# Kernel tuning notes

Measured on AMD Instinct MI355X. Metric: run time of the kernel, lower is better.

The kernel has to match this reference:

```python
import jax, jax.numpy as jnp
import numpy as np

B = 1
T_DIM, H_DIM, W_DIM = 8, 24, 24          # video canvas (t, h, w)
TT, TH, TW = 2, 8, 8                      # tile sizes
WT, WH, WW = 6, 16, 16                    # window sizes (tokens)
HIDDEN = 1024
HEADS = 16
DH = HIDDEN // HEADS
SEQ = T_DIM * H_DIM * W_DIM               # 4608
NT, NH, NW = T_DIM // TT, H_DIM // TH, W_DIM // TW   # tile grid (4,3,3)
N_TILES = NT * NH * NW                    # 36
TILE = TT * TH * TW                       # 128


def _gather_indices():
    # STA tile mask: kv tile allowed iff |clamp(q_tile, k//2, n-1-k//2) - kv_tile| <= k//2 per axis.
    # Due to the clamp, every query tile attends to exactly the same number of kv tiles,
    # so the block-sparse pattern is a dense gather of shape [N_TILES, K].
    def axis(n, kernel_tiles):
        half = kernel_tiles // 2
        c = np.clip(np.arange(n), half, n - 1 - half)
        return c[:, None] + np.arange(-half, half + 1)[None, :]  # [n, 2*half+1]
    ts = axis(NT, WT // TT)
    hs = axis(NH, WH // TH)
    ws = axis(NW, WW // TW)
    idx = (ts[:, None, None, :, None, None] * NH
           + hs[None, :, None, None, :, None]) * NW \
          + ws[None, None, :, None, None, :]
    return idx.reshape(N_TILES, -1).astype(np.int32)  # [N_TILES, K]


def setup_inputs() -> dict:
    key = jax.random.key(0)
    k1, k2, k3, k4, k5 = jax.random.split(key, 5)
    s = 0.02
    return {
        "hidden_states": jax.random.normal(k1, (B, SEQ, HIDDEN), jnp.float32),
        "q_w": jax.random.normal(k2, (HIDDEN, HIDDEN), jnp.float32) * s,
        "k_w": jax.random.normal(k3, (HIDDEN, HIDDEN), jnp.float32) * s,
        "v_w": jax.random.normal(k4, (HIDDEN, HIDDEN), jnp.float32) * s,
        "o_w": jax.random.normal(k5, (HIDDEN, HIDDEN), jnp.float32) * s,
    }


def _tileize(x):
    # [B, S, HEADS*DH] -> [B, HEADS, N_TILES, TILE, DH] in (t,h,w) tile-major order
    x = x.reshape(B, NT, TT, NH, TH, NW, TW, HEADS, DH)
    x = x.transpose(0, 7, 1, 3, 5, 2, 4, 6, 8)
    return x.reshape(B, HEADS, N_TILES, TILE, DH)


def _untileize(x):
    # [B, HEADS, N_TILES, TILE, DH] -> [B, S, HEADS*DH]
    x = x.reshape(B, HEADS, NT, NH, NW, TT, TH, TW, DH)
    x = x.transpose(0, 2, 5, 3, 6, 4, 7, 1, 8)
    return x.reshape(B, SEQ, HEADS * DH)


def reference(hidden_states, q_w, k_w, v_w, o_w):
    q = _tileize(hidden_states @ q_w.T)
    k = _tileize(hidden_states @ k_w.T)
    v = _tileize(hidden_states @ v_w.T)
    idx = jnp.asarray(_gather_indices())          # [N_TILES, K] (static)
    kk = k[:, :, idx]                              # [B, H, N_TILES, K, TILE, DH]
    vv = v[:, :, idx]
    K = idx.shape[1]
    kk = kk.reshape(B, HEADS, N_TILES, K * TILE, DH)
    vv = vv.reshape(B, HEADS, N_TILES, K * TILE, DH)
    scale = 1.0 / np.sqrt(DH).astype(np.float32)
    scores = jnp.einsum('bhnqd,bhnkd->bhnqk', q * scale, kk)  # [B,H,nT,TILE,K*TILE]
    attn = jax.nn.softmax(scores, axis=-1)
    out = jnp.einsum('bhnqk,bhnkd->bhnqd', attn, vv)
    return _untileize(out) @ o_w.T
```

## Files before the change

kernel.cpp:

```cpp
#include <hip/hip_runtime.h>
#include <math.h>

#define HID 1024
#define NHEADS 16
#define NTILES 36
#define HEADSZ (36*128*64)
#define LOG2E 1.4426950408889634f
#define PLSTRIDE 73728

typedef unsigned short u16;
typedef unsigned int u32;
typedef __attribute__((ext_vector_type(8))) u16 ushort8v;
typedef __attribute__((ext_vector_type(8))) __bf16 bf16x8;
typedef __attribute__((ext_vector_type(16))) float f32x16;
typedef __attribute__((ext_vector_type(4))) u32 u32x4;

__device__ __forceinline__ u32 cvt_pk_bf16(float lo, float hi) {
  u32 r;
  asm("v_cvt_pk_bf16_f32 %0, %1, %2" : "=v"(r) : "v"(lo), "v"(hi));
  return r;
}
__device__ __forceinline__ void permlane32_swap(u32 &a, u32 &b) {
  asm volatile("v_permlane32_swap_b32 %0, %1" : "+v"(a), "+v"(b));
}
__device__ __forceinline__ void gld_lds16(const void* g, void* l) {
  __builtin_amdgcn_global_load_lds((const __attribute__((address_space(1))) u32*)g,
                                   (__attribute__((address_space(3))) u32*)l, 16, 0, 0);
}
__device__ __forceinline__ f32x16 mfma32(bf16x8 a, bf16x8 b, f32x16 c) {
  return __builtin_amdgcn_mfma_f32_32x32x16_bf16(a, b, c, 0, 0, 0);
}
__device__ __forceinline__ u16 bf16r(float x) {
  u32 b = __builtin_bit_cast(u32, x);
  b += 0x7fff + ((b >> 16) & 1);
  return (u16)(b >> 16);
}
__device__ __forceinline__ float bf2f(u16 v) {
  return __builtin_bit_cast(float, (u32)v << 16);
}

struct CastJob { const float* src[5]; u16* dst[5]; int n[5]; };

__global__ __launch_bounds__(256)
void cast_bf16(CastJob j) {
  const int w = blockIdx.y;
  const int n = j.n[w];
  const int i = (blockIdx.x * 256 + threadIdx.x) * 8;
  if (i >= n) return;
  const float4 v0 = *reinterpret_cast<const float4*>(j.src[w] + i);
  const float4 v1 = *reinterpret_cast<const float4*>(j.src[w] + i + 4);
  u32x4 o;
  o.x = cvt_pk_bf16(v0.x, v0.y);
  o.y = cvt_pk_bf16(v0.z, v0.w);
  o.z = cvt_pk_bf16(v1.x, v1.y);
  o.w = cvt_pk_bf16(v1.z, v1.w);
  *reinterpret_cast<u32x4*>(j.dst[w] + i) = o;
}

template<int AMODE, int CMODE, bool QKV, bool DBUF>
__global__ __launch_bounds__(256)
void gemm_mfma(const u16* __restrict__ A, const u16* __restrict__ B,
               void* __restrict__ Cv, float alpha)
{
    __shared__ __align__(16) u16 sm[DBUF ? 2 : 1][2][8192];

    const int tid = threadIdx.x;
    const int wv = tid >> 6, l = tid & 63;
    const int l31 = l & 31, hi = l >> 5;
    const int wm = wv >> 1, wn = wv & 1;
    const int by = blockIdx.y;
    const int n0 = blockIdx.x * 128;
    const float av = (QKV && n0 >= 1024) ? 1.0f : alpha;

    const int tt = by / 9, rem = by % 9, th = rem / 3, tw = rem % 3;
    const int tilebase = tt * 1152 + th * 192 + tw * 8;

    const int lrow = l >> 3;
    const int lslot = l & 7;
    const int sg = (lslot ^ lrow) * 8;
    const u16* aptr[4];
    const u16* bptr[4];
#pragma unroll
    for (int i = 0; i < 4; ++i) {
        const int row = (wv * 4 + i) * 8 + lrow;
        if (AMODE == 0) {
            const int s = tilebase + (row >> 6) * 576 + ((row >> 3) & 7) * 24 + (row & 7);
            aptr[i] = A + (size_t)s * HID + sg;
        } else {
            aptr[i] = A + (size_t)(by * 128 + row) * 64 + sg;
        }
        bptr[i] = B + (size_t)(n0 + row) * HID + sg;
    }

    auto stage = [&](int buf, int kc) {
#pragma unroll
        for (int i = 0; i < 4; ++i) {
            const u16* ga = (AMODE == 0) ? (aptr[i] + kc)
                                         : (aptr[i] + (size_t)(kc >> 6) * HEADSZ);
            gld_lds16(ga, &sm[buf][0][(wv * 4 + i) * 512]);
            gld_lds16(bptr[i] + kc, &sm[buf][1][(wv * 4 + i) * 512]);
        }
    };

    f32x16 acc[2][2];
#pragma unroll
    for (int mb = 0; mb < 2; ++mb)
#pragma unroll
        for (int nb = 0; nb < 2; ++nb)
#pragma unroll
            for (int i = 0; i < 16; ++i) acc[mb][nb][i] = 0.f;

    auto compute = [&](int buf) {
        __builtin_amdgcn_s_setprio(1);
#pragma unroll
        for (int kk = 0; kk < 4; ++kk) {
            bf16x8 af[2], bfr[2];
#pragma unroll
            for (int mb = 0; mb < 2; ++mb) {
                const int row = wm * 64 + mb * 32 + l31;
                af[mb] = *reinterpret_cast<const bf16x8*>(
                    &sm[buf][0][row * 64 + (((kk * 2 + hi) ^ (row & 7)) * 8)]);
            }
#pragma unroll
            for (int nb = 0; nb < 2; ++nb) {
                const int row = wn * 64 + nb * 32 + l31;
                bfr[nb] = *reinterpret_cast<const bf16x8*>(
                    &sm[buf][1][row * 64 + (((kk * 2 + hi) ^ (row & 7)) * 8)]);
            }
#pragma unroll
            for (int mb = 0; mb < 2; ++mb)
#pragma unroll
                for (int nb = 0; nb < 2; ++nb)
                    acc[mb][nb] = mfma32(af[mb], bfr[nb], acc[mb][nb]);
        }
        __builtin_amdgcn_s_setprio(0);
    };

    if (DBUF) {
        stage(0, 0);
        __syncthreads();
        int cur = 0;
        for (int kc = 0; kc < HID; kc += 64) {
            if (kc + 64 < HID) stage(cur ^ 1, kc + 64);
            compute(cur);
            __syncthreads();
            cur ^= 1;
        }
    } else {
        for (int kc = 0; kc < HID; kc += 64) {
            __syncthreads();
            stage(0, kc);
            __syncthreads();
            compute(0);
        }
    }

    if (CMODE == 0) {
        float* C = (float*)Cv;
#pragma unroll
        for (int mb = 0; mb < 2; ++mb)
#pragma unroll
            for (int r = 0; r < 16; ++r) {
                const int m = wm * 64 + mb * 32 + (r & 3) + 8 * (r >> 2) + 4 * hi;
                const int s = tilebase + (m >> 6) * 576 + ((m >> 3) & 7) * 24 + (m & 7);
#pragma unroll
                for (int nb = 0; nb < 2; ++nb) {
                    const int n = n0 + wn * 64 + nb * 32 + l31;
                    C[(size_t)s * HID + n] = acc[mb][nb][r] * av;
                }
            }
    } else {
        u16* C = (u16*)Cv;
#pragma unroll
        for (int mb = 0; mb < 2; ++mb)
#pragma unroll
            for (int rq = 0; rq < 4; ++rq) {
                const int mbase = wm * 64 + mb * 32 + 8 * rq + 4 * hi;
#pragma unroll
                for (int nb = 0; nb < 2; ++nb) {
                    const int n = n0 + wn * 64 + nb * 32 + l31;
                    const int head = n >> 6, dh = n & 63;
                    if (QKV && head >= 32) {
                        u32 w0 = cvt_pk_bf16(acc[mb][nb][rq * 4 + 0], acc[mb][nb][rq * 4 + 1]);
                        u32 w1 = cvt_pk_bf16(acc[mb][nb][rq * 4 + 2], acc[mb][nb][rq * 4 + 3]);
                        *reinterpret_cast<uint2*>(C + (size_t)head * HEADSZ +
                            (size_t)by * 8192 + dh * 128 + mbase) = make_uint2(w0, w1);
                    } else {
#pragma unroll
                        for (int j = 0; j < 4; ++j) {
                            const int m = mbase + j;
                            C[(size_t)head * HEADSZ + (size_t)(by * 128 + m) * 64 + dh] =
                                bf16r(acc[mb][nb][rq * 4 + j] * av);
                        }
                    }
                }
            }
    }
}

__global__ __launch_bounds__(256, 5)
void attn_mfma(const u16* __restrict__ Q, const u16* __restrict__ K,
               const u16* __restrict__ Vt, u16* __restrict__ pO0,
               u16* __restrict__ pO1, float* __restrict__ pl)
{
    __shared__ u16 sm[2][2][4096];

    const int tid = threadIdx.x;
    const int wave = tid >> 6;
    const int lane = tid & 63;
    const int l31 = lane & 31;
    const int hi  = lane >> 5;

    const int logical = (blockIdx.x & 7) * 144 + (blockIdx.x >> 3);
    const int p  = logical & 1;
    const int bt = logical >> 1;
    const int tl = bt % NTILES;
    const int hd = bt / NTILES;
    const size_t headbase = (size_t)hd * HEADSZ;

    const u16* Qg = Q + headbase + (size_t)tl * 8192;
    const u16* Kh = K + headbase;
    const u16* Vh = Vt + headbase;

    bf16x8 qf[4];
    {
        const u16* qrow = Qg + (wave * 32 + l31) * 64 + hi * 8;
#pragma unroll
        for (int ks = 0; ks < 4; ++ks)
            qf[ks] = *reinterpret_cast<const bf16x8*>(qrow + ks * 16);
    }

    const int base_t = (min(max(tl / 9, 1), 2) - 1) * 9;

    const int srow = lane >> 3;
    const int slot = lane & 7;

    auto stage = [&](int i, int bi) {
        const int kt = base_t + i;
        const u16* Kg = Kh + (size_t)kt * 8192 + p * 4096;
        const u16* Vg = Vh + (size_t)kt * 8192 + p * 64;
        u16* dk = &sm[bi][0][0];
        u16* dv = &sm[bi][1][0];
#pragma unroll
        for (int q = 0; q < 2; ++q) {
            const int seg = wave * 2 + q;
            const int key = seg * 8 + srow;
            gld_lds16(Kg + key * 64 + ((slot ^ (key & 7)) * 8), dk + seg * 512);
            const int dh = seg * 8 + srow;
            gld_lds16(Vg + dh * 128 + ((slot ^ (dh & 7)) * 8), dv + seg * 512);
        }
    };

    f32x16 accO0, accO1;
#pragma unroll
    for (int i = 0; i < 16; ++i) { accO0[i] = 0.f; accO1[i] = 0.f; }
    float lsum = 0.f;

    stage(0, 0);
    __syncthreads();

    for (int i = 0; i < 27; ++i) {
        const int cur = i & 1;
        if (i + 1 < 27) stage(i + 1, cur ^ 1);
        const u16* Ksb = &sm[cur][0][0];
        const u16* Vsb = &sm[cur][1][0];

#pragma unroll
        for (int c = 0; c < 2; ++c) {
            f32x16 s;
#pragma unroll
            for (int i2 = 0; i2 < 16; ++i2) s[i2] = 0.f;
            const int kr = c * 32 + l31;
            __builtin_amdgcn_s_setprio(1);
#pragma unroll
            for (int ks = 0; ks < 4; ++ks) {
                bf16x8 a = *reinterpret_cast<const bf16x8*>(
                    Ksb + kr * 64 + (((2 * ks + hi) ^ (kr & 7)) * 8));
                s = mfma32(a, qf[ks], s);
            }
            __builtin_amdgcn_s_setprio(0);

#pragma unroll
            for (int i2 = 0; i2 < 16; ++i2) s[i2] = __builtin_amdgcn_exp2f(s[i2]);

            float ps = 0.f;
#pragma unroll
            for (int i2 = 0; i2 < 16; ++i2) ps += s[i2];
            lsum += ps;

            bf16x8 pb[2];
            {
                u32 a0 = cvt_pk_bf16(s[0], s[1]);
                u32 a1 = cvt_pk_bf16(s[2], s[3]);
                u32 b0 = cvt_pk_bf16(s[4], s[5]);
                u32 b1 = cvt_pk_bf16(s[6], s[7]);
                permlane32_swap(a0, b0);
                permlane32_swap(a1, b1);
                u32x4 w; w.x = a0; w.y = a1; w.z = b0; w.w = b1;
                pb[0] = __builtin_bit_cast(bf16x8, w);
                u32 c0 = cvt_pk_bf16(s[8], s[9]);
                u32 c1 = cvt_pk_bf16(s[10], s[11]);
                u32 d0 = cvt_pk_bf16(s[12], s[13]);
                u32 d1 = cvt_pk_bf16(s[14], s[15]);
                permlane32_swap(c0, d0);
                permlane32_swap(c1, d1);
                u32x4 w2; w2.x = c0; w2.y = c1; w2.z = d0; w2.w = d1;
                pb[1] = __builtin_bit_cast(bf16x8, w2);
            }

            __builtin_amdgcn_s_setprio(1);
#pragma unroll
            for (int k2 = 0; k2 < 2; ++k2) {
                const int sg2 = c * 4 + k2 * 2 + hi;
                bf16x8 v0 = *reinterpret_cast<const bf16x8*>(
                    Vsb + l31 * 64 + ((sg2 ^ (l31 & 7)) * 8));
                accO0 = mfma32(v0, pb[k2], accO0);
                bf16x8 v1 = *reinterpret_cast<const bf16x8*>(
                    Vsb + (32 + l31) * 64 + ((sg2 ^ (l31 & 7)) * 8));
                accO1 = mfma32(v1, pb[k2], accO1);
            }
            __builtin_amdgcn_s_setprio(0);
        }
        __syncthreads();
    }

    lsum += __shfl_xor(lsum, 32);

    u16* Ob = (p ? pO1 : pO0) + ((size_t)bt * 128 + wave * 32 + l31) * 64;
#pragma unroll
    for (int t = 0; t < 4; ++t) {
        u32 p0 = cvt_pk_bf16(accO0[4 * t], accO0[4 * t + 1]);
        u32 p1 = cvt_pk_bf16(accO0[4 * t + 2], accO0[4 * t + 3]);
        *reinterpret_cast<uint2*>(Ob + t * 8 + 4 * hi) = make_uint2(p0, p1);
        u32 q0 = cvt_pk_bf16(accO1[4 * t], accO1[4 * t + 1]);
        u32 q1 = cvt_pk_bf16(accO1[4 * t + 2], accO1[4 * t + 3]);
        *reinterpret_cast<uint2*>(Ob + 32 + t * 8 + 4 * hi) = make_uint2(q0, q1);
    }
    if (hi == 0) pl[p * PLSTRIDE + bt * 128 + wave * 32 + l31] = lsum;
}

__global__ __launch_bounds__(256)
void merge_attn(const u16* __restrict__ pO0, const u16* __restrict__ pO1,
                const float* __restrict__ pl, u16* __restrict__ O)
{
    const int b = blockIdx.x;
    const int tid = threadIdx.x;
    const int row = tid >> 1;
    const int d0 = (tid & 1) * 32;
    const size_t rbase = ((size_t)b * 128 + row) * 64 + d0;
    const float inv = 1.f / (pl[b * 128 + row] + pl[PLSTRIDE + b * 128 + row]);
#pragma unroll
    for (int g = 0; g < 4; ++g) {
        ushort8v a = *reinterpret_cast<const ushort8v*>(pO0 + rbase + g * 8);
        ushort8v c = *reinterpret_cast<const ushort8v*>(pO1 + rbase + g * 8);
        u32 w[4];
#pragma unroll
        for (int h = 0; h < 4; ++h) {
            float f0 = (bf2f(a[2 * h])     + bf2f(c[2 * h]))     * inv;
            float f1 = (bf2f(a[2 * h + 1]) + bf2f(c[2 * h + 1])) * inv;
            w[h] = cvt_pk_bf16(f0, f1);
        }
        u32x4 st; st.x = w[0]; st.y = w[1]; st.z = w[2]; st.w = w[3];
        *reinterpret_cast<u32x4*>(O + rbase + g * 8) = st;
    }
}

extern "C" void kernel_launch(void* const* d_in, const int* in_sizes, int n_in,
                              void* d_out, int out_size, void* d_ws, size_t ws_size,
                              hipStream_t stream) {
    const float* hs = (const float*)d_in[0];
    const float* qw = (const float*)d_in[1];
    const float* kw = (const float*)d_in[2];
    const float* vw = (const float*)d_in[3];
    const float* ow = (const float*)d_in[4];
    float* out = (float*)d_out;

    const size_t TSZ = (size_t)NHEADS * HEADSZ;
    const size_t WSZ = (size_t)HID * HID;
    u16* hsb = (u16*)d_ws;
    u16* wqb = hsb + TSZ;
    u16* wkb = wqb + WSZ;
    u16* wvb = wkb + WSZ;
    u16* wob = wvb + WSZ;
    u16* qb  = wob + WSZ;
    u16* kb  = qb + TSZ;
    u16* vt  = kb + TSZ;
    u16* pO0 = hsb;
    u16* pO1 = vt + TSZ;
    float* pl = (float*)(pO1 + TSZ);
    u16* aob = (u16*)(pl + 2 * PLSTRIDE);

    CastJob cj;
    cj.src[0] = hs; cj.dst[0] = hsb; cj.n[0] = (int)TSZ;
    cj.src[1] = qw; cj.dst[1] = wqb; cj.n[1] = (int)WSZ;
    cj.src[2] = kw; cj.dst[2] = wkb; cj.n[2] = (int)WSZ;
    cj.src[3] = vw; cj.dst[3] = wvb; cj.n[3] = (int)WSZ;
    cj.src[4] = ow; cj.dst[4] = wob; cj.n[4] = (int)WSZ;
    cast_bf16<<<dim3(2304, 5), 256, 0, stream>>>(cj);

    gemm_mfma<0, 1, true, true><<<dim3(24, 36), 256, 0, stream>>>(hsb, wqb, qb, 0.125f * LOG2E);
    attn_mfma<<<NHEADS * NTILES * 2, 256, 0, stream>>>(qb, kb, vt, pO0, pO1, pl);
    merge_attn<<<NHEADS * NTILES, 256, 0, stream>>>(pO0, pO1, pl, aob);
    gemm_mfma<1, 0, false, true><<<dim3(8, 36), 256, 0, stream>>>(aob, wob, out, 1.0f);
}
```

Measured before the change: 158.6 us.

## Split attention waves over query and key halves, reduce partial outputs through LDS

The 4 waves in each attention block are regrouped as a 2x2 grid. Each wave now handles 64 query rows against 32 of the 64 keys in a stage, instead of 32 query rows against all 64 keys. Each K fragment loaded from LDS now feeds two query blocks, and each V fragment feeds two accumulators, which roughly halves per-wave LDS reads per MFMA. The two key-half waves then combine their partial outputs and row sums through an LDS reduction after the loop. In exchange the kernel holds more accumulator and Q registers, drops the occupancy hint from 5 to 3 blocks, and adds an extra barrier and epilogue pass.

```diff
diff --git a/kernel.cpp b/kernel.cpp
--- a/kernel.cpp
+++ b/kernel.cpp
@@ -198,18 +198,21 @@
     }
 }
 
-__global__ __launch_bounds__(256, 5)
+__global__ __launch_bounds__(256, 3)
 void attn_mfma(const u16* __restrict__ Q, const u16* __restrict__ K,
                const u16* __restrict__ Vt, u16* __restrict__ pO0,
                u16* __restrict__ pO1, float* __restrict__ pl)
 {
     __shared__ u16 sm[2][2][4096];
+    __shared__ float lsl[2][2][32];
 
     const int tid = threadIdx.x;
     const int wave = tid >> 6;
     const int lane = tid & 63;
     const int l31 = lane & 31;
     const int hi  = lane >> 5;
+    const int qw  = wave & 1;
+    const int kw  = wave >> 1;
 
     const int logical = (blockIdx.x & 7) * 144 + (blockIdx.x >> 3);
     const int p  = logical & 1;
@@ -222,12 +225,13 @@
     const u16* Kh = K + headbase;
     const u16* Vh = Vt + headbase;
 
-    bf16x8 qf[4];
-    {
-        const u16* qrow = Qg + (wave * 32 + l31) * 64 + hi * 8;
+    bf16x8 qf[2][4];
+#pragma unroll
+    for (int qb = 0; qb < 2; ++qb) {
+        const u16* qrow = Qg + (qw * 64 + qb * 32 + l31) * 64 + hi * 8;
 #pragma unroll
         for (int ks = 0; ks < 4; ++ks)
-            qf[ks] = *reinterpret_cast<const bf16x8*>(qrow + ks * 16);
+            qf[qb][ks] = *reinterpret_cast<const bf16x8*>(qrow + ks * 16);
     }
 
     const int base_t = (min(max(tl / 9, 1), 2) - 1) * 9;
@@ -251,13 +255,19 @@
         }
     };
 
-    f32x16 accO0, accO1;
-#pragma unroll
-    for (int i = 0; i < 16; ++i) { accO0[i] = 0.f; accO1[i] = 0.f; }
-    float lsum = 0.f;
+    f32x16 accO[2][2];
+#pragma unroll
+    for (int dhb = 0; dhb < 2; ++dhb)
+#pragma unroll
+        for (int qb = 0; qb < 2; ++qb)
+#pragma unroll
+            for (int i = 0; i < 16; ++i) accO[dhb][qb][i] = 0.f;
+    float lsum[2] = {0.f, 0.f};
 
     stage(0, 0);
     __syncthreads();
+
+    const int kr = kw * 32 + l31;
 
     for (int i = 0; i < 27; ++i) {
         const int cur = i & 1;
@@ -265,19 +275,22 @@
         const u16* Ksb = &sm[cur][0][0];
         const u16* Vsb = &sm[cur][1][0];
 
-#pragma unroll
-        for (int c = 0; c < 2; ++c) {
+        bf16x8 af[4];
+#pragma unroll
+        for (int ks = 0; ks < 4; ++ks)
+            af[ks] = *reinterpret_cast<const bf16x8*>(
+                Ksb + kr * 64 + (((2 * ks + hi) ^ (kr & 7)) * 8));
+
+        bf16x8 pb[2][2];
+#pragma unroll
+        for (int qb = 0; qb < 2; ++qb) {
             f32x16 s;
 #pragma unroll
             for (int i2 = 0; i2 < 16; ++i2) s[i2] = 0.f;
-            const int kr = c * 32 + l31;
             __builtin_amdgcn_s_setprio(1);
 #pragma unroll
-            for (int ks = 0; ks < 4; ++ks) {
-                bf16x8 a = *reinterpret_cast<const bf16x8*>(
-                    Ksb + kr * 64 + (((2 * ks + hi) ^ (kr & 7)) * 8));
-                s = mfma32(a, qf[ks], s);
-            }
+            for (int ks = 0; ks < 4; ++ks)
+                s = mfma32(af[ks], qf[qb][ks], s);
             __builtin_amdgcn_s_setprio(0);
 
 #pragma unroll
@@ -286,57 +299,99 @@
             float ps = 0.f;
 #pragma unroll
             for (int i2 = 0; i2 < 16; ++i2) ps += s[i2];
-            lsum += ps;
-
-            bf16x8 pb[2];
-            {
-                u32 a0 = cvt_pk_bf16(s[0], s[1]);
-                u32 a1 = cvt_pk_bf16(s[2], s[3]);
-                u32 b0 = cvt_pk_bf16(s[4], s[5]);
-                u32 b1 = cvt_pk_bf16(s[6], s[7]);
-                permlane32_swap(a0, b0);
-                permlane32_swap(a1, b1);
-                u32x4 w; w.x = a0; w.y = a1; w.z = b0; w.w = b1;
-                pb[0] = __builtin_bit_cast(bf16x8, w);
-                u32 c0 = cvt_pk_bf16(s[8], s[9]);
-                u32 c1 = cvt_pk_bf16(s[10], s[11]);
-                u32 d0 = cvt_pk_bf16(s[12], s[13]);
-                u32 d1 = cvt_pk_bf16(s[14], s[15]);
-                permlane32_swap(c0, d0);
-                permlane32_swap(c1, d1);
-                u32x4 w2; w2.x = c0; w2.y = c1; w2.z = d0; w2.w = d1;
-                pb[1] = __builtin_bit_cast(bf16x8, w2);
-            }
-
-            __builtin_amdgcn_s_setprio(1);
-#pragma unroll
-            for (int k2 = 0; k2 < 2; ++k2) {
-                const int sg2 = c * 4 + k2 * 2 + hi;
-                bf16x8 v0 = *reinterpret_cast<const bf16x8*>(
-                    Vsb + l31 * 64 + ((sg2 ^ (l31 & 7)) * 8));
-                accO0 = mfma32(v0, pb[k2], accO0);
-                bf16x8 v1 = *reinterpret_cast<const bf16x8*>(
-                    Vsb + (32 + l31) * 64 + ((sg2 ^ (l31 & 7)) * 8));
-                accO1 = mfma32(v1, pb[k2], accO1);
-            }
-            __builtin_amdgcn_s_setprio(0);
-        }
+            lsum[qb] += ps;
+
+            u32 a0 = cvt_pk_bf16(s[0], s[1]);
+            u32 a1 = cvt_pk_bf16(s[2], s[3]);
+            u32 b0 = cvt_pk_bf16(s[4], s[5]);
+            u32 b1 = cvt_pk_bf16(s[6], s[7]);
+            permlane32_swap(a0, b0);
+            permlane32_swap(a1, b1);
+            u32x4 w; w.x = a0; w.y = a1; w.z = b0; w.w = b1;
+            pb[qb][0] = __builtin_bit_cast(bf16x8, w);
+            u32 c0 = cvt_pk_bf16(s[8], s[9]);
+            u32 c1 = cvt_pk_bf16(s[10], s[11]);
+            u32 d0 = cvt_pk_bf16(s[12], s[13]);
+            u32 d1 = cvt_pk_bf16(s[14], s[15]);
+            permlane32_swap(c0, d0);
+            permlane32_swap(c1, d1);
+            u32x4 w2; w2.x = c0; w2.y = c1; w2.z = d0; w2.w = d1;
+            pb[qb][1] = __builtin_bit_cast(bf16x8, w2);
+        }
+
+        __builtin_amdgcn_s_setprio(1);
+#pragma unroll
+        for (int k2 = 0; k2 < 2; ++k2) {
+            const int sg2 = kw * 4 + k2 * 2 + hi;
+            bf16x8 v0 = *reinterpret_cast<const bf16x8*>(
+                Vsb + l31 * 64 + ((sg2 ^ (l31 & 7)) * 8));
+            bf16x8 v1 = *reinterpret_cast<const bf16x8*>(
+                Vsb + (32 + l31) * 64 + ((sg2 ^ ((32 + l31) & 7)) * 8));
+            accO[0][0] = mfma32(v0, pb[0][k2], accO[0][0]);
+            accO[1][0] = mfma32(v1, pb[0][k2], accO[1][0]);
+            accO[0][1] = mfma32(v0, pb[1][k2], accO[0][1]);
+            accO[1][1] = mfma32(v1, pb[1][k2], accO[1][1]);
+        }
+        __builtin_amdgcn_s_setprio(0);
         __syncthreads();
     }
 
-    lsum += __shfl_xor(lsum, 32);
-
-    u16* Ob = (p ? pO1 : pO0) + ((size_t)bt * 128 + wave * 32 + l31) * 64;
-#pragma unroll
-    for (int t = 0; t < 4; ++t) {
-        u32 p0 = cvt_pk_bf16(accO0[4 * t], accO0[4 * t + 1]);
-        u32 p1 = cvt_pk_bf16(accO0[4 * t + 2], accO0[4 * t + 3]);
-        *reinterpret_cast<uint2*>(Ob + t * 8 + 4 * hi) = make_uint2(p0, p1);
-        u32 q0 = cvt_pk_bf16(accO1[4 * t], accO1[4 * t + 1]);
-        u32 q1 = cvt_pk_bf16(accO1[4 * t + 2], accO1[4 * t + 3]);
-        *reinterpret_cast<uint2*>(Ob + 32 + t * 8 + 4 * hi) = make_uint2(q0, q1);
-    }
-    if (hi == 0) pl[p * PLSTRIDE + bt * 128 + wave * 32 + l31] = lsum;
+    lsum[0] += __shfl_xor(lsum[0], 32);
+    lsum[1] += __shfl_xor(lsum[1], 32);
+
+    float* fs = reinterpret_cast<float*>(&sm[0][0][0]);
+    if (kw == 1) {
+#pragma unroll
+        for (int dhb = 0; dhb < 2; ++dhb)
+#pragma unroll
+            for (int qb = 0; qb < 2; ++qb)
+#pragma unroll
+                for (int r4 = 0; r4 < 4; ++r4) {
+                    const int c = (dhb * 2 + qb) * 4 + r4;
+                    float4 v = make_float4(accO[dhb][qb][4 * r4 + 0],
+                                           accO[dhb][qb][4 * r4 + 1],
+                                           accO[dhb][qb][4 * r4 + 2],
+                                           accO[dhb][qb][4 * r4 + 3]);
+                    *reinterpret_cast<float4*>(&fs[qw * 4096 + c * 256 + lane * 4]) = v;
+                }
+        if (hi == 0) { lsl[qw][0][l31] = lsum[0]; lsl[qw][1][l31] = lsum[1]; }
+    }
+    __syncthreads();
+    if (kw == 0) {
+#pragma unroll
+        for (int dhb = 0; dhb < 2; ++dhb)
+#pragma unroll
+            for (int qb = 0; qb < 2; ++qb)
+#pragma unroll
+                for (int r4 = 0; r4 < 4; ++r4) {
+                    const int c = (dhb * 2 + qb) * 4 + r4;
+                    float4 v = *reinterpret_cast<const float4*>(
+                        &fs[qw * 4096 + c * 256 + lane * 4]);
+                    accO[dhb][qb][4 * r4 + 0] += v.x;
+                    accO[dhb][qb][4 * r4 + 1] += v.y;
+                    accO[dhb][qb][4 * r4 + 2] += v.z;
+                    accO[dhb][qb][4 * r4 + 3] += v.w;
+                }
+        lsum[0] += lsl[qw][0][l31];
+        lsum[1] += lsl[qw][1][l31];
+
+        u16* Ob = (p ? pO1 : pO0) + ((size_t)(bt * 128 + qw * 64)) * 64;
+#pragma unroll
+        for (int qb = 0; qb < 2; ++qb)
+#pragma unroll
+            for (int dhb = 0; dhb < 2; ++dhb)
+#pragma unroll
+                for (int t = 0; t < 4; ++t) {
+                    u32 w0 = cvt_pk_bf16(accO[dhb][qb][4 * t + 0], accO[dhb][qb][4 * t + 1]);
+                    u32 w1 = cvt_pk_bf16(accO[dhb][qb][4 * t + 2], accO[dhb][qb][4 * t + 3]);
+                    *reinterpret_cast<uint2*>(Ob + (qb * 32 + l31) * 64 +
+                                              dhb * 32 + t * 8 + 4 * hi) = make_uint2(w0, w1);
+                }
+        if (hi == 0) {
+            pl[p * PLSTRIDE + bt * 128 + qw * 64 + l31]      = lsum[0];
+            pl[p * PLSTRIDE + bt * 128 + qw * 64 + 32 + l31] = lsum[1];
+        }
+    }
 }
 
 __global__ __launch_bounds__(256)
```

Measured after the change: 197.7 us. +24.7%, slower.

## Fuse split-KV merge into output projection GEMM with smaller M tiles

Applied to the files above, without the earlier changes.

Removes the separate merge_attn kernel and folds the two-partial softmax merge (sum of partials times reciprocal of combined row sums) into the A-operand load of a new output-projection GEMM. The new GEMM reads the per-head partial outputs directly, merges them in registers, writes them to LDS, and uses 64-row tiles giving a 8x72 grid. This avoids one launch and a full intermediate write and read. In exchange the A path now uses plain register loads instead of direct-to-LDS loads, and each block fetches two partial buffers plus row sums for every k-chunk.

```diff
diff --git a/kernel.cpp b/kernel.cpp
--- a/kernel.cpp
+++ b/kernel.cpp
@@ -195,6 +195,126 @@
                     }
                 }
             }
+    }
+}
+
+__global__ __launch_bounds__(256)
+void gemm_out(const u16* __restrict__ P0, const u16* __restrict__ P1,
+              const float* __restrict__ PL, const u16* __restrict__ B,
+              float* __restrict__ C)
+{
+    __shared__ __align__(16) u16 smA[2][4096];
+    __shared__ __align__(16) u16 smB[2][8192];
+
+    const int tid = threadIdx.x;
+    const int wv = tid >> 6, l = tid & 63;
+    const int l31 = l & 31, hi = l >> 5;
+    const int wm = wv >> 1, wn = wv & 1;
+    const int by = blockIdx.y;
+    const int n0 = blockIdx.x * 128;
+
+    const int tile = by >> 1;
+    const int tt = tile / 9, rem = tile % 9, th = rem / 3, tw = rem % 3;
+    const int tilebase = tt * 1152 + th * 192 + tw * 8;
+
+    const int lrow = l >> 3;
+    const int lslot = l & 7;
+    const int sg = (lslot ^ lrow) * 8;
+
+    const u16* bptr[4];
+#pragma unroll
+    for (int i = 0; i < 4; ++i) {
+        const int row = (wv * 4 + i) * 8 + lrow;
+        bptr[i] = B + (size_t)(n0 + row) * HID + sg;
+    }
+    int arow[2];
+#pragma unroll
+    for (int i = 0; i < 2; ++i) arow[i] = (wv * 2 + i) * 8 + lrow;
+
+    auto stageB = [&](int buf, int kc) {
+#pragma unroll
+        for (int i = 0; i < 4; ++i)
+            gld_lds16(bptr[i] + kc, &smB[buf][(wv * 4 + i) * 512]);
+    };
+
+    ushort8v a0[2], a1[2];
+    float ls[2];
+    auto loadA = [&](int kc) {
+        const int head = kc >> 6;
+#pragma unroll
+        for (int i = 0; i < 2; ++i) {
+            const size_t gb = (size_t)head * HEADSZ +
+                              (size_t)(by * 64 + arow[i]) * 64 + sg;
+            a0[i] = *reinterpret_cast<const ushort8v*>(P0 + gb);
+            a1[i] = *reinterpret_cast<const ushort8v*>(P1 + gb);
+            const int pli = head * 4608 + by * 64 + arow[i];
+            ls[i] = PL[pli] + PL[PLSTRIDE + pli];
+        }
+    };
+    auto mergeA = [&](int buf) {
+#pragma unroll
+        for (int i = 0; i < 2; ++i) {
+            const float r = __builtin_amdgcn_rcpf(ls[i]);
+            u32 w[4];
+#pragma unroll
+            for (int h = 0; h < 4; ++h) {
+                float f0 = (bf2f(a0[i][2 * h])     + bf2f(a1[i][2 * h]))     * r;
+                float f1 = (bf2f(a0[i][2 * h + 1]) + bf2f(a1[i][2 * h + 1])) * r;
+                w[h] = cvt_pk_bf16(f0, f1);
+            }
+            u32x4 st; st.x = w[0]; st.y = w[1]; st.z = w[2]; st.w = w[3];
+            *reinterpret_cast<u32x4*>(&smA[buf][(wv * 2 + i) * 512 + l * 8]) = st;
+        }
+    };
+
+    f32x16 acc[2];
+#pragma unroll
+    for (int nb = 0; nb < 2; ++nb)
+#pragma unroll
+        for (int i = 0; i < 16; ++i) acc[nb][i] = 0.f;
+
+    auto compute = [&](int buf) {
+        __builtin_amdgcn_s_setprio(1);
+#pragma unroll
+        for (int kk = 0; kk < 4; ++kk) {
+            const int ar = wm * 32 + l31;
+            bf16x8 af = *reinterpret_cast<const bf16x8*>(
+                &smA[buf][ar * 64 + (((kk * 2 + hi) ^ (ar & 7)) * 8)]);
+#pragma unroll
+            for (int nb = 0; nb < 2; ++nb) {
+                const int brow = wn * 64 + nb * 32 + l31;
+                bf16x8 bf_ = *reinterpret_cast<const bf16x8*>(
+                    &smB[buf][brow * 64 + (((kk * 2 + hi) ^ (brow & 7)) * 8)]);
+                acc[nb] = mfma32(af, bf_, acc[nb]);
+            }
+        }
+        __builtin_amdgcn_s_setprio(0);
+    };
+
+    loadA(0);
+    stageB(0, 0);
+    mergeA(0);
+    __syncthreads();
+    int cur = 0;
+    for (int kc = 0; kc < HID; kc += 64) {
+        const bool more = (kc + 64 < HID);
+        if (more) { loadA(kc + 64); stageB(cur ^ 1, kc + 64); }
+        compute(cur);
+        if (more) mergeA(cur ^ 1);
+        __syncthreads();
+        cur ^= 1;
+    }
+
+#pragma unroll
+    for (int r = 0; r < 16; ++r) {
+        const int m = wm * 32 + (r & 3) + 8 * (r >> 2) + 4 * hi;
+        const int r128 = (by & 1) * 64 + m;
+        const int s = tilebase + (r128 >> 6) * 576 + ((r128 >> 3) & 7) * 24 + (r128 & 7);
+#pragma unroll
+        for (int nb = 0; nb < 2; ++nb) {
+            const int n = n0 + wn * 64 + nb * 32 + l31;
+            C[(size_t)s * HID + n] = acc[nb][r];
+        }
     }
 }
 
@@ -339,32 +459,6 @@
     if (hi == 0) pl[p * PLSTRIDE + bt * 128 + wave * 32 + l31] = lsum;
 }
 
-__global__ __launch_bounds__(256)
-void merge_attn(const u16* __restrict__ pO0, const u16* __restrict__ pO1,
-                const float* __restrict__ pl, u16* __restrict__ O)
-{
-    const int b = blockIdx.x;
-    const int tid = threadIdx.x;
-    const int row = tid >> 1;
-    const int d0 = (tid & 1) * 32;
-    const size_t rbase = ((size_t)b * 128 + row) * 64 + d0;
-    const float inv = 1.f / (pl[b * 128 + row] + pl[PLSTRIDE + b * 128 + row]);
-#pragma unroll
-    for (int g = 0; g < 4; ++g) {
-        ushort8v a = *reinterpret_cast<const ushort8v*>(pO0 + rbase + g * 8);
-        ushort8v c = *reinterpret_cast<const ushort8v*>(pO1 + rbase + g * 8);
-        u32 w[4];
-#pragma unroll
-        for (int h = 0; h < 4; ++h) {
-            float f0 = (bf2f(a[2 * h])     + bf2f(c[2 * h]))     * inv;
-            float f1 = (bf2f(a[2 * h + 1]) + bf2f(c[2 * h + 1])) * inv;
-            w[h] = cvt_pk_bf16(f0, f1);
-        }
-        u32x4 st; st.x = w[0]; st.y = w[1]; st.z = w[2]; st.w = w[3];
-        *reinterpret_cast<u32x4*>(O + rbase + g * 8) = st;
-    }
-}
-
 extern "C" void kernel_launch(void* const* d_in, const int* in_sizes, int n_in,
                               void* d_out, int out_size, void* d_ws, size_t ws_size,
                               hipStream_t stream) {
@@ -388,7 +482,6 @@
     u16* pO0 = hsb;
     u16* pO1 = vt + TSZ;
     float* pl = (float*)(pO1 + TSZ);
-    u16* aob = (u16*)(pl + 2 * PLSTRIDE);
 
     CastJob cj;
     cj.src[0] = hs; cj.dst[0] = hsb; cj.n[0] = (int)TSZ;
@@ -400,6 +493,5 @@
 
     gemm_mfma<0, 1, true, true><<<dim3(24, 36), 256, 0, stream>>>(hsb, wqb, qb, 0.125f * LOG2E);
     attn_mfma<<<NHEADS * NTILES * 2, 256, 0, stream>>>(qb, kb, vt, pO0, pO1, pl);
-    merge_attn<<<NHEADS * NTILES, 256, 0, stream>>>(pO0, pO1, pl, aob);
-    gemm_mfma<1, 0, false, true><<<dim3(8, 36), 256, 0, stream>>>(aob, wob, out, 1.0f);
-}
+    gemm_out<<<dim3(8, 72), 256, 0, stream>>>(pO0, pO1, pl, wob, out);
+}
```

Result: slower. 163.8 us (+3.3%).
